# Performance work log

Measured on AMD Instinct MI355X. Metric: run time of the kernel, lower is better.

Reference implementation:

```python
import jax, jax.numpy as jnp
import numpy as np
from functools import partial

C = 10   # number of regular-repr fields
G = 4    # C4 rotation group order
EPS = 1e-5


def _lift_kernel(w):
    """Lifting (trivial->regular) P4 kernel. w: [C, Cin, k, k] ->
    full kernel [C*G, Cin, k, k] with output channel layout (field, orientation)."""
    ks = [jnp.rot90(w, r, axes=(-2, -1)) for r in range(G)]  # each [C,Cin,k,k]
    k = jnp.stack(ks, axis=1)                                 # [C,G,Cin,k,k]
    return k.reshape(w.shape[0] * G, w.shape[1], w.shape[2], w.shape[3])


def _gconv_kernel(w):
    """Regular->regular P4 kernel. w: [Cout, Cin, G, k, k] (indexed by relative
    input orientation) -> full kernel [Cout*G, Cin*G, k, k].
    K[co*G+r, ci*G+s] = rot90(w[co, ci, (s-r) mod G], r)."""
    Cout, Cin, _, k1, k2 = w.shape
    ks = []
    for r in range(G):
        wr = jnp.roll(w, shift=r, axis=2)             # wr[..., s, :, :] = w[..., (s-r)%G]
        wr = jnp.rot90(wr, r, axes=(-2, -1))          # rotate spatially by r*90deg
        ks.append(wr)
    k = jnp.stack(ks, axis=1)                          # [Cout, G, Cin, G, k, k]
    return k.reshape(Cout * G, Cin * G, k1, k2)


def _conv(x, k, pad):
    return jax.lax.conv_general_dilated(
        x, k, window_strides=(1, 1), padding=pad,
        dimension_numbers=('NCHW', 'OIHW', 'NCHW'))


def _bn_relu(x, gamma, beta):
    """InnerBatchNorm (stats shared over the G orientations of each field) + ReLU."""
    B, CG, H, W = x.shape
    xr = x.reshape(B, C, G, H, W)
    m = xr.mean(axis=(0, 2, 3, 4), keepdims=True)
    v = xr.var(axis=(0, 2, 3, 4), keepdims=True)
    g = gamma[None, :, None, None, None]
    b = beta[None, :, None, None, None]
    y = (xr - m) * jax.lax.rsqrt(v + EPS) * g + b
    return jnp.maximum(y.reshape(B, CG, H, W), 0.0)


def _maxpool2(x):
    return jax.lax.reduce_window(x, -jnp.inf, jax.lax.max,
                                 (1, 1, 2, 2), (1, 1, 2, 2), 'VALID')


def setup_inputs() -> dict:
    key = jax.random.key(0)
    ks = jax.random.split(key, 20)
    B = 1024
    x = jax.random.normal(ks[0], (B, 1, 28, 28), dtype=jnp.float32)
    w1 = jax.random.normal(ks[1], (C, 1, 3, 3), dtype=jnp.float32) * 0.3
    w2 = jax.random.normal(ks[2], (C, C, G, 3, 3), dtype=jnp.float32) * 0.1
    w3 = jax.random.normal(ks[3], (C, C, G, 3, 3), dtype=jnp.float32) * 0.1
    w4 = jax.random.normal(ks[4], (C, C, G, 3, 3), dtype=jnp.float32) * 0.1
    w5 = jax.random.normal(ks[5], (C, C, G, 3, 3), dtype=jnp.float32) * 0.1
    w6 = jax.random.normal(ks[6], (C, C, G, 3, 3), dtype=jnp.float32) * 0.1
    w7 = jax.random.normal(ks[7], (C, C, G, 4, 4), dtype=jnp.float32) * 0.1
    g1 = jnp.ones((C,), jnp.float32) + 0.1 * jax.random.normal(ks[8], (C,))
    b1 = 0.1 * jax.random.normal(ks[9], (C,))
    g2 = jnp.ones((C,), jnp.float32) + 0.1 * jax.random.normal(ks[10], (C,))
    b2 = 0.1 * jax.random.normal(ks[11], (C,))
    gs = jnp.ones((C,), jnp.float32) + 0.1 * jax.random.normal(ks[12], (C,))
    bs = 0.1 * jax.random.normal(ks[13], (C,))
    wfc = jax.random.normal(ks[14], (10, C * 11 * 11), dtype=jnp.float32) * 0.05
    bfc = jnp.zeros((10,), jnp.float32)
    return dict(x=x, w1=w1, w2=w2, w3=w3, w4=w4, w5=w5, w6=w6, w7=w7,
                g1=g1, b1=b1, g2=g2, b2=b2, gs=gs, bs=bs, wfc=wfc, bfc=bfc)


PAD1 = [(1, 1), (1, 1)]
PAD0 = [(0, 0), (0, 0)]


def reference(x, w1, w2, w3, w4, w5, w6, w7, g1, b1, g2, b2, gs, bs, wfc, bfc):
    # block1: lifting P4 conv 3x3 pad1 + InnerBN + ReLU  -> [B, 40, 28, 28]
    h = _bn_relu(_conv(x, _lift_kernel(w1), PAD1), g1, b1)
    # block2: P4 conv + BN + ReLU + 2x2 max pool         -> [B, 40, 14, 14]
    h = _maxpool2(_bn_relu(_conv(h, _gconv_kernel(w2), PAD1), g2, b2))
    # blocks 3-6: P4 conv + shared BN/ReLU               -> [B, 40, 14, 14]
    for w in (w3, w4, w5, w6):
        h = _bn_relu(_conv(h, _gconv_kernel(w), PAD1), gs, bs)
    # block7: P4 conv 4x4 pad0 + shared BN/ReLU          -> [B, 40, 11, 11]
    h = _bn_relu(_conv(h, _gconv_kernel(w7), PAD0), gs, bs)
    # group pooling: max over the G orientations of each field -> [B, 10, 11, 11]
    B = h.shape[0]
    h = h.reshape(B, C, G, 11, 11).max(axis=2)
    # fc
    return h.reshape(B, -1) @ wfc.T + bfc
```

## Files before the change

kernel.cpp:

```cpp
#include <hip/hip_runtime.h>

#define EPSV 1e-5f
#define INV28 (1.f / 3211264.f)
#define INV14 (1.f / 802816.f)
#define INV11 (1.f / 495616.f)

typedef __bf16 v8bf __attribute__((ext_vector_type(8)));
typedef _Float16 v8h __attribute__((ext_vector_type(8)));
typedef _Float16 v4h __attribute__((ext_vector_type(4)));
typedef float v4f __attribute__((ext_vector_type(4)));

__device__ __forceinline__ int rotsrc(int r, int dy, int dx, int K) {
  int sy, sx;
  if (r == 0)      { sy = dy;       sx = dx; }
  else if (r == 1) { sy = dx;       sx = K - 1 - dy; }
  else if (r == 2) { sy = K - 1 - dy; sx = K - 1 - dx; }
  else             { sy = K - 1 - dx; sx = dy; }
  return sy * K + sx;
}

__device__ __forceinline__ float gw_val(const float* __restrict__ w, int oc, int g,
                                        int j, int KS) {
  int tap = g / 5, cig = g % 5, ci = cig * 8 + j;
  int co = oc >> 2, r = oc & 3, cin = ci >> 2, s = ci & 3;
  int srel = (s - r) & 3;
  return w[((co * 10 + cin) * 4 + srel) * (KS * KS) + rotsrc(r, tap / KS, tap % KS, KS)];
}

__device__ __forceinline__ float stat8a(const float* __restrict__ p, int i) {
  float v = 0.f;
#pragma unroll
  for (int c = 0; c < 8; ++c)
    v += __hip_atomic_load(&p[c * 32 + i], __ATOMIC_RELAXED, __HIP_MEMORY_SCOPE_AGENT);
  return v;
}

__global__ void prep_kernel(const float* __restrict__ w1, const float* __restrict__ w2,
                            const float* __restrict__ w3, const float* __restrict__ w4,
                            const float* __restrict__ w5, const float* __restrict__ w6,
                            const float* __restrict__ w7,
                            float* __restrict__ K1, __bf16* __restrict__ Wb,
                            float* __restrict__ stats) {
  int idx = blockIdx.x * blockDim.x + threadIdx.x;
  if (idx < 1792) { stats[idx] = 0.f; return; }
  idx -= 1792;
  if (idx < 360) {
    int tap = idx / 40, oc = idx % 40;
    int c = oc >> 2, r = oc & 3;
    K1[idx] = w1[c * 9 + rotsrc(r, tap / 3, tap % 3, 3)];
    return;
  }
  idx -= 360;
  if (idx < 92160) {
    int l = idx / 18432, r0 = idx % 18432;
    const float* w = (l == 0) ? w2 : (l == 1) ? w3 : (l == 2) ? w4 : (l == 3) ? w5 : w6;
    int mt = r0 / 6144, r1 = r0 % 6144;
    int c = r1 / 512, r2 = r1 % 512;
    int q = r2 / 128, r3 = r2 % 128;
    int ocl = r3 / 8, j = r3 % 8;
    int oc = mt * 16 + ocl, g = c * 4 + q;
    float val = 0.f;
    if (oc < 40 && g < 45) val = gw_val(w, oc, g, j, 3);
    Wb[idx] = (__bf16)val;
    return;
  }
  idx -= 92160;
  if (idx < 30720) {
    int mt = idx / 10240, r1 = idx % 10240;
    int c = r1 / 512, r2 = r1 % 512;
    int q = r2 / 128, r3 = r2 % 128;
    int ocl = r3 / 8, j = r3 % 8;
    int oc = mt * 16 + ocl, g = c * 4 + q;
    float val = 0.f;
    if (oc < 40) val = gw_val(w7, oc, g, j, 4);
    Wb[92160 + idx] = (__bf16)val;
  }
}

__global__ __launch_bounds__(256) void conv1_stats(
    const float* __restrict__ x, const float* __restrict__ K1,
    float* __restrict__ stats) {
  __shared__ float ximg[900];
  __shared__ float wk[360];
  __shared__ float sstat[20];
  const int tid = threadIdx.x, img = blockIdx.x;
  if (tid < 20) sstat[tid] = 0.f;
  for (int i = tid; i < 900; i += 256) {
    int gy = i / 30 - 1, gx = i % 30 - 1;
    ximg[i] = (gy >= 0 && gy < 28 && gx >= 0 && gx < 28)
                  ? x[img * 784 + gy * 28 + gx] : 0.f;
  }
  for (int i = tid; i < 360; i += 256) wk[i] = K1[i];
  __syncthreads();

  float s[10], q[10];
#pragma unroll
  for (int f = 0; f < 10; ++f) { s[f] = 0.f; q[f] = 0.f; }
  for (int p = tid; p < 784; p += 256) {
    const int y = p / 28, xx = p % 28;
    float patch[9];
#pragma unroll
    for (int t = 0; t < 9; ++t) patch[t] = ximg[(y + t / 3) * 30 + xx + t % 3];
#pragma unroll
    for (int f = 0; f < 10; ++f) {
#pragma unroll
      for (int r = 0; r < 4; ++r) {
        const int oc = f * 4 + r;
        float v = 0.f;
#pragma unroll
        for (int t = 0; t < 9; ++t) v = fmaf(patch[t], wk[t * 40 + oc], v);
        s[f] += v; q[f] += v * v;
      }
    }
  }
#pragma unroll
  for (int f = 0; f < 10; ++f) {
#pragma unroll
    for (int off = 1; off <= 32; off <<= 1) {
      s[f] += __shfl_xor(s[f], off, 64);
      q[f] += __shfl_xor(q[f], off, 64);
    }
  }
  if ((tid & 63) == 0) {
#pragma unroll
    for (int f = 0; f < 10; ++f) {
      atomicAdd(&sstat[f], s[f]);
      atomicAdd(&sstat[10 + f], q[f]);
    }
  }
  __syncthreads();
  if (tid < 20) atomicAdd(&stats[(img & 7) * 32 + tid], sstat[tid]);
}

template<int R>
__global__ __launch_bounds__(256) void conv_band_fused(
    const float* __restrict__ x, const float* __restrict__ K1,
    const __bf16* __restrict__ Wl, const float* __restrict__ pstats,
    const float* __restrict__ pgamma, const float* __restrict__ pbeta,
    float pinvn, _Float16* __restrict__ T0, float* __restrict__ stats) {
  constexpr int NPIX = R * 28, NSUB = NPIX / 16, NSW = (NSUB + 3) / 4;
  constexpr int SROWS = R + 2, XR = R + 4;
  __shared__ __attribute__((aligned(16))) __bf16 tile[SROWS * 30 * 40];
  __shared__ float xpatch[XR * 32];
  __shared__ float wk[360];
  __shared__ float sc[10], sh[10], sstat[20];
  const int tid = threadIdx.x;
  int img, y0;
  if constexpr (R == 8) { img = blockIdx.x / 3; y0 = (blockIdx.x % 3) * 8; }
  else { img = blockIdx.x; y0 = 24; }

  if (tid < 20) sstat[tid] = 0.f;
  if (tid >= 32 && tid < 42) {
    int f = tid - 32;
    float mu = stat8a(pstats, f) * pinvn, q = stat8a(pstats, 10 + f) * pinvn;
    float isd = rsqrtf(q - mu * mu + EPSV);
    float s = pgamma[f] * isd;
    sc[f] = s; sh[f] = pbeta[f] - mu * s;
  }
  for (int i = tid; i < XR * 32; i += 256) {
    int gy = y0 - 2 + i / 32, gx = i % 32 - 2;
    xpatch[i] = (gy >= 0 && gy < 28 && gx >= 0 && gx < 28)
                    ? x[(long)img * 784 + gy * 28 + gx] : 0.f;
  }
  for (int i = tid; i < 360; i += 256) wk[i] = K1[i];
  __syncthreads();

  for (int p = tid; p < SROWS * 30; p += 256) {
    const int iy = p / 30, ix = p % 30;
    const int gy = y0 + iy - 1, gx = ix - 1;
    const bool inb = (gy >= 0 && gy < 28 && gx >= 0 && gx < 28);
    float patch[9];
#pragma unroll
    for (int t = 0; t < 9; ++t)
      patch[t] = xpatch[(iy + t / 3) * 32 + ix + t % 3];
    __bf16* tb = &tile[p * 40];
    if (inb) {
#pragma unroll 8
      for (int ci = 0; ci < 40; ++ci) {
        float v = 0.f;
#pragma unroll
        for (int t = 0; t < 9; ++t) v = fmaf(patch[t], wk[t * 40 + ci], v);
        v = fmaxf(0.f, fmaf(v, sc[ci >> 2], sh[ci >> 2]));
        tb[ci] = (__bf16)v;
      }
    } else {
#pragma unroll 8
      for (int ci = 0; ci < 40; ++ci) tb[ci] = (__bf16)0.f;
    }
  }
  __syncthreads();

  const int lane = tid & 63, wv = tid >> 6;
  const int m = lane & 15, quad = lane >> 4;
  int pbase[NSW], nsv[NSW];
  bool sv[NSW];
#pragma unroll
  for (int s = 0; s < NSW; ++s) {
    int ns = wv + 4 * s;
    sv[s] = ns < NSUB;
    int n = ns * 16 + m;
    n = n < NPIX ? n : NPIX - 1;
    nsv[s] = n;
    pbase[s] = ((n / 28) * 30 + (n % 28)) * 40;
  }
  v4f acc[3][NSW] = {};

  const __bf16* wlane = Wl + (quad * 16 + m) * 8;
  for (int c = 0; c < 12; ++c) {
    int g = 4 * c + quad; g = g > 44 ? 44 : g;
    int tap = g / 5, cig = g - tap * 5;
    int boff = ((tap / 3) * 30 + (tap % 3)) * 40 + cig * 8;
    v8bf bfr[NSW];
#pragma unroll
    for (int s = 0; s < NSW; ++s)
      if (sv[s]) bfr[s] = *(const v8bf*)&tile[pbase[s] + boff];
    v8bf afr[3];
#pragma unroll
    for (int mt = 0; mt < 3; ++mt)
      afr[mt] = *(const v8bf*)(wlane + (mt * 12 + c) * 512);
#pragma unroll
    for (int s = 0; s < NSW; ++s)
      if (sv[s]) {
#pragma unroll
        for (int mt = 0; mt < 3; ++mt)
          acc[mt][s] = __builtin_amdgcn_mfma_f32_16x16x32_bf16(afr[mt], bfr[s],
                                                              acc[mt][s], 0, 0, 0);
      }
  }

#pragma unroll
  for (int mt = 0; mt < 3; ++mt) {
    float svv = 0.f, qvv = 0.f;
#pragma unroll
    for (int s = 0; s < NSW; ++s)
      if (sv[s]) {
#pragma unroll
        for (int r = 0; r < 4; ++r) { float v = acc[mt][s][r]; svv += v; qvv += v * v; }
      }
    const bool ocok = (mt < 2) || (quad < 2);
#pragma unroll
    for (int off = 1; off <= 8; off <<= 1) {
      svv += __shfl_xor(svv, off, 64);
      qvv += __shfl_xor(qvv, off, 64);
    }
    if (m == 0 && ocok) {
      atomicAdd(&sstat[mt * 4 + quad], svv);
      atomicAdd(&sstat[10 + mt * 4 + quad], qvv);
    }
  }

  __syncthreads();
  __bf16* pool = tile;
#pragma unroll
  for (int mt = 0; mt < 3; ++mt) {
    const bool ocok = (mt < 2) || (quad < 2);
    const int oc0 = mt * 16 + quad * 4;
#pragma unroll
    for (int s = 0; s < NSW; ++s)
      if (ocok && sv[s]) {
#pragma unroll
        for (int r = 0; r < 4; ++r)
          pool[(oc0 + r) * NPIX + nsv[s]] = (__bf16)acc[mt][s][r];
      }
  }
  __syncthreads();
  constexpr int PR = R / 2, PCNT = 40 * PR * 14;
  for (int i = tid; i < PCNT; i += 256) {
    int oc = i / (PR * 14), rem = i % (PR * 14);
    int py = rem / 14, px = rem % 14;
    const __bf16* pp = pool + oc * NPIX + py * 56 + px * 2;
    float a = (float)pp[0], b = (float)pp[1], c = (float)pp[28], d = (float)pp[29];
    T0[((long)img * 256 + (y0 / 2 + py + 1) * 16 + (px + 1)) * 40 + oc] =
        (_Float16)fmaxf(fmaxf(a, b), fmaxf(c, d));
  }
  if (tid < 20) atomicAdd(&stats[(img & 7) * 32 + tid], sstat[tid]);
}

__global__ __launch_bounds__(256) void conv_tile(
    const _Float16* __restrict__ Tin, const __bf16* __restrict__ Wl,
    const float* __restrict__ pstats, const float* __restrict__ pg,
    const float* __restrict__ pb, float pinvn,
    _Float16* __restrict__ Tout, float* __restrict__ stG) {
  __shared__ __attribute__((aligned(16))) __bf16 tile[256 * 40];
  __shared__ float sc[10], sh[10], sstat[20];
  const int tid = threadIdx.x, img = blockIdx.x;
  const int lane = tid & 63, wv = tid >> 6;
  const int m = lane & 15, quad = lane >> 4;
  if (tid < 20) sstat[tid] = 0.f;
  if (tid >= 32 && tid < 42) {
    int f = tid - 32;
    float mu = stat8a(pstats, f) * pinvn, q = stat8a(pstats, 10 + f) * pinvn;
    float isd = rsqrtf(q - mu * mu + EPSV);
    float s = pg[f] * isd;
    sc[f] = s; sh[f] = pb[f] - mu * s;
  }
  __syncthreads();
  {
    const int iy = tid >> 4, ix = tid & 15;
    const bool border = (iy == 0) | (iy == 15) | (ix == 0) | (ix == 15);
    const _Float16* src = Tin + ((long)img * 256 + tid) * 40;
    __bf16* dst = &tile[tid * 40];
#pragma unroll
    for (int cg5 = 0; cg5 < 5; ++cg5) {
      v8bf pk;
      if (!border) {
        v8h rv = *(const v8h*)(src + cg5 * 8);
#pragma unroll
        for (int u = 0; u < 8; ++u) {
          const int f = (cg5 * 8 + u) >> 2;
          pk[u] = (__bf16)fmaxf(0.f, fmaf((float)rv[u], sc[f], sh[f]));
        }
      } else {
#pragma unroll
        for (int u = 0; u < 8; ++u) pk[u] = (__bf16)0.f;
      }
      *(v8bf*)(dst + cg5 * 8) = pk;
    }
  }
  __syncthreads();

  int pb3[4], n3[4];
  bool sv3[4], va3[4];
#pragma unroll
  for (int s = 0; s < 4; ++s) {
    int ns = wv + 4 * s;
    sv3[s] = ns < 13;
    int n = ns * 16 + m;
    va3[s] = sv3[s] && (n < 196);
    n = n < 196 ? n : 195;
    n3[s] = n;
    pb3[s] = ((n / 14) * 16 + (n % 14)) * 40;
  }
  const int wofs = (quad * 16 + m) * 8;
  v4f acc[3][4];
#pragma unroll
  for (int mt = 0; mt < 3; ++mt)
#pragma unroll
    for (int s = 0; s < 4; ++s) acc[mt][s] = (v4f){0.f, 0.f, 0.f, 0.f};
  for (int c = 0; c < 12; ++c) {
    int g = 4 * c + quad; g = g > 44 ? 44 : g;
    int tap = g / 5, cig = g - tap * 5;
    int boff = ((tap / 3) * 16 + (tap % 3)) * 40 + cig * 8;
    v8bf bfr[4];
#pragma unroll
    for (int s = 0; s < 4; ++s)
      if (sv3[s]) bfr[s] = *(const v8bf*)&tile[pb3[s] + boff];
    v8bf afr[3];
#pragma unroll
    for (int mt = 0; mt < 3; ++mt)
      afr[mt] = *(const v8bf*)(Wl + wofs + (mt * 12 + c) * 512);
#pragma unroll
    for (int s = 0; s < 4; ++s)
      if (sv3[s]) {
#pragma unroll
        for (int mt = 0; mt < 3; ++mt)
          acc[mt][s] = __builtin_amdgcn_mfma_f32_16x16x32_bf16(afr[mt], bfr[s],
                                                              acc[mt][s], 0, 0, 0);
      }
  }

#pragma unroll
  for (int mt = 0; mt < 3; ++mt) {
    float svv = 0.f, qvv = 0.f;
#pragma unroll
    for (int s = 0; s < 4; ++s)
      if (va3[s]) {
#pragma unroll
        for (int r = 0; r < 4; ++r) { float v = acc[mt][s][r]; svv += v; qvv += v * v; }
      }
    const bool ocok = (mt < 2) || (quad < 2);
#pragma unroll
    for (int off = 1; off <= 8; off <<= 1) {
      svv += __shfl_xor(svv, off, 64);
      qvv += __shfl_xor(qvv, off, 64);
    }
    if (m == 0 && ocok) {
      atomicAdd(&sstat[mt * 4 + quad], svv);
      atomicAdd(&sstat[10 + mt * 4 + quad], qvv);
    }
  }
  __syncthreads();
  if (tid < 20) atomicAdd(&stG[(img & 7) * 32 + tid], sstat[tid]);

#pragma unroll
  for (int mt = 0; mt < 3; ++mt) {
    const bool ocok = (mt < 2) || (quad < 2);
    if (!ocok) continue;
#pragma unroll
    for (int s = 0; s < 4; ++s)
      if (va3[s]) {
        v4h pk;
#pragma unroll
        for (int r = 0; r < 4; ++r) pk[r] = (_Float16)acc[mt][s][r];
        const int n = n3[s];
        *(v4h*)(Tout + ((long)img * 256 + (n / 14 + 1) * 16 + (n % 14 + 1)) * 40
                + mt * 16 + quad * 4) = pk;
      }
  }
}

__global__ __launch_bounds__(256) void conv7_tile(
    const _Float16* __restrict__ Tin, const __bf16* __restrict__ Wl,
    const float* __restrict__ pstats, const float* __restrict__ pg,
    const float* __restrict__ pb,
    _Float16* __restrict__ T7, float* __restrict__ stG) {
  __shared__ __attribute__((aligned(16))) __bf16 tile[256 * 40];
  __shared__ float sc[10], sh[10], sstat[20];
  const int tid = threadIdx.x, img = blockIdx.x;
  const int lane = tid & 63, wv = tid >> 6;
  const int m = lane & 15, quad = lane >> 4;
  if (tid < 20) sstat[tid] = 0.f;
  if (tid >= 32 && tid < 42) {
    int f = tid - 32;
    float mu = stat8a(pstats, f) * INV14, q = stat8a(pstats, 10 + f) * INV14;
    float isd = rsqrtf(q - mu * mu + EPSV);
    float s = pg[f] * isd;
    sc[f] = s; sh[f] = pb[f] - mu * s;
  }
  __syncthreads();
  {
    const int iy = tid >> 4, ix = tid & 15;
    const bool border = (iy == 0) | (iy == 15) | (ix == 0) | (ix == 15);
    const _Float16* src = Tin + ((long)img * 256 + tid) * 40;
    __bf16* dst = &tile[tid * 40];
#pragma unroll
    for (int cg5 = 0; cg5 < 5; ++cg5) {
      v8bf pk;
      if (!border) {
        v8h rv = *(const v8h*)(src + cg5 * 8);
#pragma unroll
        for (int u = 0; u < 8; ++u) {
          const int f = (cg5 * 8 + u) >> 2;
          pk[u] = (__bf16)fmaxf(0.f, fmaf((float)rv[u], sc[f], sh[f]));
        }
      } else {
#pragma unroll
        for (int u = 0; u < 8; ++u) pk[u] = (__bf16)0.f;
      }
      *(v8bf*)(dst + cg5 * 8) = pk;
    }
  }
  __syncthreads();

  int pb7[2], n7[2];
  bool va7[2];
#pragma unroll
  for (int s = 0; s < 2; ++s) {
    int ns = wv + 4 * s;
    int n = ns * 16 + m;
    va7[s] = n < 121;
    n = n < 121 ? n : 120;
    n7[s] = n;
    pb7[s] = ((n / 11 + 1) * 16 + (n % 11 + 1)) * 40;
  }
  const int wofs = (quad * 16 + m) * 8;
  v4f acc[3][2];
#pragma unroll
  for (int mt = 0; mt < 3; ++mt)
#pragma unroll
    for (int s = 0; s < 2; ++s) acc[mt][s] = (v4f){0.f, 0.f, 0.f, 0.f};
  for (int c = 0; c < 20; ++c) {
    int g = 4 * c + quad;
    int tap = g / 5, cig = g - tap * 5;
    int boff = ((tap >> 2) * 16 + (tap & 3)) * 40 + cig * 8;
    v8bf bfr[2];
#pragma unroll
    for (int s = 0; s < 2; ++s) bfr[s] = *(const v8bf*)&tile[pb7[s] + boff];
    v8bf afr[3];
#pragma unroll
    for (int mt = 0; mt < 3; ++mt)
      afr[mt] = *(const v8bf*)(Wl + wofs + (mt * 20 + c) * 512);
#pragma unroll
    for (int s = 0; s < 2; ++s)
#pragma unroll
      for (int mt = 0; mt < 3; ++mt)
        acc[mt][s] = __builtin_amdgcn_mfma_f32_16x16x32_bf16(afr[mt], bfr[s],
                                                            acc[mt][s], 0, 0, 0);
  }

#pragma unroll
  for (int mt = 0; mt < 3; ++mt) {
    float svv = 0.f, qvv = 0.f;
#pragma unroll
    for (int s = 0; s < 2; ++s)
      if (va7[s]) {
#pragma unroll
        for (int r = 0; r < 4; ++r) { float v = acc[mt][s][r]; svv += v; qvv += v * v; }
      }
    const bool ocok = (mt < 2) || (quad < 2);
#pragma unroll
    for (int off = 1; off <= 8; off <<= 1) {
      svv += __shfl_xor(svv, off, 64);
      qvv += __shfl_xor(qvv, off, 64);
    }
    if (m == 0 && ocok) {
      atomicAdd(&sstat[mt * 4 + quad], svv);
      atomicAdd(&sstat[10 + mt * 4 + quad], qvv);
    }
  }
  __syncthreads();
  if (tid < 20) atomicAdd(&stG[(img & 7) * 32 + tid], sstat[tid]);

#pragma unroll
  for (int mt = 0; mt < 3; ++mt) {
    const bool ocok = (mt < 2) || (quad < 2);
    if (!ocok) continue;
#pragma unroll
    for (int s = 0; s < 2; ++s)
      if (va7[s]) {
        v4h pk;
#pragma unroll
        for (int r = 0; r < 4; ++r) pk[r] = (_Float16)acc[mt][s][r];
        *(v4h*)(T7 + ((long)img * 121 + n7[s]) * 40 + mt * 16 + quad * 4) = pk;
      }
  }
}

__global__ __launch_bounds__(256) void head_kernel(
    const _Float16* __restrict__ T7, const float* __restrict__ stats7,
    const float* __restrict__ gs, const float* __restrict__ bs,
    const float* __restrict__ wfc, const float* __restrict__ bfc,
    float* __restrict__ out) {
  __shared__ float sc[10], sh[10];
  __shared__ float mbuf[1210];
  __shared__ float red[40];
  const int tid = threadIdx.x, img = blockIdx.x;
  if (tid < 10) {
    float mu = stat8a(stats7, tid) * INV11, q = stat8a(stats7, 10 + tid) * INV11;
    float isd = rsqrtf(q - mu * mu + EPSV);
    float s = gs[tid] * isd;
    sc[tid] = s;
    sh[tid] = bs[tid] - mu * s;
  }
  __syncthreads();
  for (int p = tid; p < 121; p += 256) {
    const _Float16* rp = T7 + ((long)img * 121 + p) * 40;
#pragma unroll
    for (int cg5 = 0; cg5 < 5; ++cg5) {
      v8h v = *(const v8h*)(rp + cg5 * 8);
#pragma unroll
      for (int fh = 0; fh < 2; ++fh) {
        const int f = cg5 * 2 + fh;
        float mx = fmaf((float)v[fh * 4], sc[f], sh[f]);
#pragma unroll
        for (int r = 1; r < 4; ++r)
          mx = fmaxf(mx, fmaf((float)v[fh * 4 + r], sc[f], sh[f]));
        mbuf[f * 121 + p] = fmaxf(0.f, mx);
      }
    }
  }
  __syncthreads();
  const int wv = tid >> 6;
  for (int k = 0; k < 10; ++k) {
    float p = 0.f;
    for (int j = tid; j < 1210; j += 256) p = fmaf(mbuf[j], wfc[k * 1210 + j], p);
#pragma unroll
    for (int off = 32; off > 0; off >>= 1) p += __shfl_xor(p, off, 64);
    if ((tid & 63) == 0) red[k * 4 + wv] = p;
  }
  __syncthreads();
  if (tid < 10)
    out[img * 10 + tid] = bfc[tid] + red[tid * 4] + red[tid * 4 + 1] +
                          red[tid * 4 + 2] + red[tid * 4 + 3];
}

extern "C" void kernel_launch(void* const* d_in, const int* in_sizes, int n_in,
                              void* d_out, int out_size, void* d_ws, size_t ws_size,
                              hipStream_t stream) {
  const float* x   = (const float*)d_in[0];
  const float* w1  = (const float*)d_in[1];
  const float* w2  = (const float*)d_in[2];
  const float* w3  = (const float*)d_in[3];
  const float* w4  = (const float*)d_in[4];
  const float* w5  = (const float*)d_in[5];
  const float* w6  = (const float*)d_in[6];
  const float* w7  = (const float*)d_in[7];
  const float* g1  = (const float*)d_in[8];
  const float* b1  = (const float*)d_in[9];
  const float* g2  = (const float*)d_in[10];
  const float* b2  = (const float*)d_in[11];
  const float* gs  = (const float*)d_in[12];
  const float* bs  = (const float*)d_in[13];
  const float* wfc = (const float*)d_in[14];
  const float* bfc = (const float*)d_in[15];

  float* ws = (float*)d_ws;
  float* K1    = ws;
  float* stats = ws + 360;
  __bf16* Wb   = (__bf16*)(ws + 2152);
  _Float16* T0 = (_Float16*)(ws + 63592);
  _Float16* T1 = (_Float16*)(ws + 5306472L);
  _Float16* T7 = (_Float16*)(ws + 10549352L);

  prep_kernel<<<489, 256, 0, stream>>>(w1, w2, w3, w4, w5, w6, w7, K1, Wb, stats);
  conv1_stats<<<1024, 256, 0, stream>>>(x, K1, stats);
  conv_band_fused<8><<<3072, 256, 0, stream>>>(x, K1, Wb, stats, g1, b1, INV28,
                                               T0, stats + 256);
  conv_band_fused<4><<<1024, 256, 0, stream>>>(x, K1, Wb, stats, g1, b1, INV28,
                                               T0, stats + 256);
  conv_tile<<<1024, 256, 0, stream>>>(T0, Wb + 18432, stats + 256, g2, b2, INV28,
                                      T1, stats + 512);
  conv_tile<<<1024, 256, 0, stream>>>(T1, Wb + 36864, stats + 512, gs, bs, INV14,
                                      T0, stats + 768);
  conv_tile<<<1024, 256, 0, stream>>>(T0, Wb + 55296, stats + 768, gs, bs, INV14,
                                      T1, stats + 1024);
  conv_tile<<<1024, 256, 0, stream>>>(T1, Wb + 73728, stats + 1024, gs, bs, INV14,
                                      T0, stats + 1280);
  conv7_tile<<<1024, 256, 0, stream>>>(T0, Wb + 92160, stats + 1280, gs, bs,
                                       T7, stats + 1536);
  head_kernel<<<1024, 256, 0, stream>>>(T7, stats + 1536, gs, bs, wfc, bfc,
                                        (float*)d_out);
}
```

Baseline: 319.5 us.

## Recompute lifting conv with fp16 MFMA and switch all gconv operands to fp16

The scalar FMA loop that recomputed the lifting conv (block1) inside the fused band kernel is replaced by an MFMA-based im2col of 9 taps zero-padded to 32, using a new packed fp16 weight matrix built in the prep kernel. All bf16 tiles, weights and MFMA calls become fp16, which also removes the fp16-to-bf16 conversion when tiles are staged. This offloads the per-pixel 360-FMA recompute to the matrix cores and shrinks shared memory. In exchange, fp16 has less exponent range than bf16, and the MFMA wastes most of its K dimension.

```diff
diff --git a/kernel.cpp b/kernel.cpp
--- a/kernel.cpp
+++ b/kernel.cpp
@@ -5,7 +5,6 @@
 #define INV14 (1.f / 802816.f)
 #define INV11 (1.f / 495616.f)
 
-typedef __bf16 v8bf __attribute__((ext_vector_type(8)));
 typedef _Float16 v8h __attribute__((ext_vector_type(8)));
 typedef _Float16 v4h __attribute__((ext_vector_type(4)));
 typedef float v4f __attribute__((ext_vector_type(4)));
@@ -39,7 +38,7 @@
                             const float* __restrict__ w3, const float* __restrict__ w4,
                             const float* __restrict__ w5, const float* __restrict__ w6,
                             const float* __restrict__ w7,
-                            float* __restrict__ K1, __bf16* __restrict__ Wb,
+                            float* __restrict__ K1, _Float16* __restrict__ Wb,
                             float* __restrict__ stats) {
   int idx = blockIdx.x * blockDim.x + threadIdx.x;
   if (idx < 1792) { stats[idx] = 0.f; return; }
@@ -61,7 +60,7 @@
     int oc = mt * 16 + ocl, g = c * 4 + q;
     float val = 0.f;
     if (oc < 40 && g < 45) val = gw_val(w, oc, g, j, 3);
-    Wb[idx] = (__bf16)val;
+    Wb[idx] = (_Float16)val;
     return;
   }
   idx -= 92160;
@@ -73,7 +72,19 @@
     int oc = mt * 16 + ocl, g = c * 4 + q;
     float val = 0.f;
     if (oc < 40) val = gw_val(w7, oc, g, j, 4);
-    Wb[92160 + idx] = (__bf16)val;
+    Wb[92160 + idx] = (_Float16)val;
+    return;
+  }
+  idx -= 30720;
+  if (idx < 1536) {
+    int mt = idx / 512, r1 = idx % 512;
+    int q = r1 / 128, r2 = r1 % 128;
+    int ocl = r2 / 8, j = r2 % 8;
+    int oc = mt * 16 + ocl, k = q * 8 + j;
+    float val = 0.f;
+    if (oc < 40 && k < 9)
+      val = w1[(oc >> 2) * 9 + rotsrc(oc & 3, k / 3, k % 3, 3)];
+    Wb[122880 + idx] = (_Float16)val;
   }
 }
 
@@ -134,15 +145,15 @@
 
 template<int R>
 __global__ __launch_bounds__(256) void conv_band_fused(
-    const float* __restrict__ x, const float* __restrict__ K1,
-    const __bf16* __restrict__ Wl, const float* __restrict__ pstats,
+    const float* __restrict__ x, const _Float16* __restrict__ W1m,
+    const _Float16* __restrict__ Wl, const float* __restrict__ pstats,
     const float* __restrict__ pgamma, const float* __restrict__ pbeta,
     float pinvn, _Float16* __restrict__ T0, float* __restrict__ stats) {
   constexpr int NPIX = R * 28, NSUB = NPIX / 16, NSW = (NSUB + 3) / 4;
   constexpr int SROWS = R + 2, XR = R + 4;
-  __shared__ __attribute__((aligned(16))) __bf16 tile[SROWS * 30 * 40];
-  __shared__ float xpatch[XR * 32];
-  __shared__ float wk[360];
+  constexpr int NPIX_S = SROWS * 30, NSUB_S = (NPIX_S + 15) / 16;
+  __shared__ __attribute__((aligned(16))) _Float16 tile[SROWS * 30 * 40];
+  __shared__ _Float16 xpatch[XR * 32];
   __shared__ float sc[10], sh[10], sstat[20];
   const int tid = threadIdx.x;
   int img, y0;
@@ -159,39 +170,59 @@
   }
   for (int i = tid; i < XR * 32; i += 256) {
     int gy = y0 - 2 + i / 32, gx = i % 32 - 2;
-    xpatch[i] = (gy >= 0 && gy < 28 && gx >= 0 && gx < 28)
-                    ? x[(long)img * 784 + gy * 28 + gx] : 0.f;
-  }
-  for (int i = tid; i < 360; i += 256) wk[i] = K1[i];
-  __syncthreads();
-
-  for (int p = tid; p < SROWS * 30; p += 256) {
-    const int iy = p / 30, ix = p % 30;
-    const int gy = y0 + iy - 1, gx = ix - 1;
-    const bool inb = (gy >= 0 && gy < 28 && gx >= 0 && gx < 28);
-    float patch[9];
-#pragma unroll
-    for (int t = 0; t < 9; ++t)
-      patch[t] = xpatch[(iy + t / 3) * 32 + ix + t % 3];
-    __bf16* tb = &tile[p * 40];
-    if (inb) {
-#pragma unroll 8
-      for (int ci = 0; ci < 40; ++ci) {
-        float v = 0.f;
-#pragma unroll
-        for (int t = 0; t < 9; ++t) v = fmaf(patch[t], wk[t * 40 + ci], v);
-        v = fmaxf(0.f, fmaf(v, sc[ci >> 2], sh[ci >> 2]));
-        tb[ci] = (__bf16)v;
-      }
-    } else {
-#pragma unroll 8
-      for (int ci = 0; ci < 40; ++ci) tb[ci] = (__bf16)0.f;
-    }
+    float v = (gy >= 0 && gy < 28 && gx >= 0 && gx < 28)
+                  ? x[(long)img * 784 + gy * 28 + gx] : 0.f;
+    xpatch[i] = (_Float16)v;
   }
   __syncthreads();
 
   const int lane = tid & 63, wv = tid >> 6;
   const int m = lane & 15, quad = lane >> 4;
+
+  {
+    v8h a1[3];
+#pragma unroll
+    for (int mt = 0; mt < 3; ++mt)
+      a1[mt] = *(const v8h*)(W1m + mt * 512 + (quad * 16 + m) * 8);
+    for (int ns = wv; ns < NSUB_S; ns += 4) {
+      const int n = ns * 16 + m;
+      const bool valid = n < NPIX_S;
+      const int nc = valid ? n : NPIX_S - 1;
+      const int iy = nc / 30, ix = nc % 30;
+      v8h bfr;
+#pragma unroll
+      for (int j = 0; j < 8; ++j) bfr[j] = (_Float16)0.f;
+      if (quad < 2) {
+#pragma unroll
+        for (int j = 0; j < 8; ++j) {
+          const int k = quad * 8 + j;
+          if (k < 9) bfr[j] = xpatch[(iy + k / 3) * 32 + (ix + k % 3)];
+        }
+      }
+      v4f cfr[3];
+#pragma unroll
+      for (int mt = 0; mt < 3; ++mt)
+        cfr[mt] = __builtin_amdgcn_mfma_f32_16x16x32_f16(
+            a1[mt], bfr, (v4f){0.f, 0.f, 0.f, 0.f}, 0, 0, 0);
+      const int gy = y0 + iy - 1, gx = ix - 1;
+      const bool inb = (gy >= 0 && gy < 28 && gx >= 0 && gx < 28);
+#pragma unroll
+      for (int mt = 0; mt < 3; ++mt) {
+        if (mt == 2 && quad >= 2) continue;
+        const int f = mt * 4 + quad;
+        const float scf = sc[f], shf = sh[f];
+        v4h pk;
+#pragma unroll
+        for (int r = 0; r < 4; ++r) {
+          float v = inb ? fmaxf(0.f, fmaf(cfr[mt][r], scf, shf)) : 0.f;
+          pk[r] = (_Float16)v;
+        }
+        if (valid) *(v4h*)&tile[nc * 40 + mt * 16 + quad * 4] = pk;
+      }
+    }
+  }
+  __syncthreads();
+
   int pbase[NSW], nsv[NSW];
   bool sv[NSW];
 #pragma unroll
@@ -205,26 +236,26 @@
   }
   v4f acc[3][NSW] = {};
 
-  const __bf16* wlane = Wl + (quad * 16 + m) * 8;
+  const _Float16* wlane = Wl + (quad * 16 + m) * 8;
   for (int c = 0; c < 12; ++c) {
     int g = 4 * c + quad; g = g > 44 ? 44 : g;
     int tap = g / 5, cig = g - tap * 5;
     int boff = ((tap / 3) * 30 + (tap % 3)) * 40 + cig * 8;
-    v8bf bfr[NSW];
+    v8h bfr[NSW];
 #pragma unroll
     for (int s = 0; s < NSW; ++s)
-      if (sv[s]) bfr[s] = *(const v8bf*)&tile[pbase[s] + boff];
-    v8bf afr[3];
+      if (sv[s]) bfr[s] = *(const v8h*)&tile[pbase[s] + boff];
+    v8h afr[3];
 #pragma unroll
     for (int mt = 0; mt < 3; ++mt)
-      afr[mt] = *(const v8bf*)(wlane + (mt * 12 + c) * 512);
+      afr[mt] = *(const v8h*)(wlane + (mt * 12 + c) * 512);
 #pragma unroll
     for (int s = 0; s < NSW; ++s)
       if (sv[s]) {
 #pragma unroll
         for (int mt = 0; mt < 3; ++mt)
-          acc[mt][s] = __builtin_amdgcn_mfma_f32_16x16x32_bf16(afr[mt], bfr[s],
-                                                              acc[mt][s], 0, 0, 0);
+          acc[mt][s] = __builtin_amdgcn_mfma_f32_16x16x32_f16(afr[mt], bfr[s],
+                                                             acc[mt][s], 0, 0, 0);
       }
   }
 
@@ -250,7 +281,7 @@
   }
 
   __syncthreads();
-  __bf16* pool = tile;
+  _Float16* pool = tile;
 #pragma unroll
   for (int mt = 0; mt < 3; ++mt) {
     const bool ocok = (mt < 2) || (quad < 2);
@@ -260,7 +291,7 @@
       if (ocok && sv[s]) {
 #pragma unroll
         for (int r = 0; r < 4; ++r)
-          pool[(oc0 + r) * NPIX + nsv[s]] = (__bf16)acc[mt][s][r];
+          pool[(oc0 + r) * NPIX + nsv[s]] = (_Float16)acc[mt][s][r];
       }
   }
   __syncthreads();
@@ -268,7 +299,7 @@
   for (int i = tid; i < PCNT; i += 256) {
     int oc = i / (PR * 14), rem = i % (PR * 14);
     int py = rem / 14, px = rem % 14;
-    const __bf16* pp = pool + oc * NPIX + py * 56 + px * 2;
+    const _Float16* pp = pool + oc * NPIX + py * 56 + px * 2;
     float a = (float)pp[0], b = (float)pp[1], c = (float)pp[28], d = (float)pp[29];
     T0[((long)img * 256 + (y0 / 2 + py + 1) * 16 + (px + 1)) * 40 + oc] =
         (_Float16)fmaxf(fmaxf(a, b), fmaxf(c, d));
@@ -277,11 +308,11 @@
 }
 
 __global__ __launch_bounds__(256) void conv_tile(
-    const _Float16* __restrict__ Tin, const __bf16* __restrict__ Wl,
+    const _Float16* __restrict__ Tin, const _Float16* __restrict__ Wl,
     const float* __restrict__ pstats, const float* __restrict__ pg,
     const float* __restrict__ pb, float pinvn,
     _Float16* __restrict__ Tout, float* __restrict__ stG) {
-  __shared__ __attribute__((aligned(16))) __bf16 tile[256 * 40];
+  __shared__ __attribute__((aligned(16))) _Float16 tile[256 * 40];
   __shared__ float sc[10], sh[10], sstat[20];
   const int tid = threadIdx.x, img = blockIdx.x;
   const int lane = tid & 63, wv = tid >> 6;
@@ -299,22 +330,22 @@
     const int iy = tid >> 4, ix = tid & 15;
     const bool border = (iy == 0) | (iy == 15) | (ix == 0) | (ix == 15);
     const _Float16* src = Tin + ((long)img * 256 + tid) * 40;
-    __bf16* dst = &tile[tid * 40];
+    _Float16* dst = &tile[tid * 40];
 #pragma unroll
     for (int cg5 = 0; cg5 < 5; ++cg5) {
-      v8bf pk;
+      v8h pk;
       if (!border) {
         v8h rv = *(const v8h*)(src + cg5 * 8);
 #pragma unroll
         for (int u = 0; u < 8; ++u) {
           const int f = (cg5 * 8 + u) >> 2;
-          pk[u] = (__bf16)fmaxf(0.f, fmaf((float)rv[u], sc[f], sh[f]));
+          pk[u] = (_Float16)fmaxf(0.f, fmaf((float)rv[u], sc[f], sh[f]));
         }
       } else {
 #pragma unroll
-        for (int u = 0; u < 8; ++u) pk[u] = (__bf16)0.f;
-      }
-      *(v8bf*)(dst + cg5 * 8) = pk;
+        for (int u = 0; u < 8; ++u) pk[u] = (_Float16)0.f;
+      }
+      *(v8h*)(dst + cg5 * 8) = pk;
     }
   }
   __syncthreads();
@@ -341,21 +372,21 @@
     int g = 4 * c + quad; g = g > 44 ? 44 : g;
     int tap = g / 5, cig = g - tap * 5;
     int boff = ((tap / 3) * 16 + (tap % 3)) * 40 + cig * 8;
-    v8bf bfr[4];
+    v8h bfr[4];
 #pragma unroll
     for (int s = 0; s < 4; ++s)
-      if (sv3[s]) bfr[s] = *(const v8bf*)&tile[pb3[s] + boff];
-    v8bf afr[3];
+      if (sv3[s]) bfr[s] = *(const v8h*)&tile[pb3[s] + boff];
+    v8h afr[3];
 #pragma unroll
     for (int mt = 0; mt < 3; ++mt)
-      afr[mt] = *(const v8bf*)(Wl + wofs + (mt * 12 + c) * 512);
+      afr[mt] = *(const v8h*)(Wl + wofs + (mt * 12 + c) * 512);
 #pragma unroll
     for (int s = 0; s < 4; ++s)
       if (sv3[s]) {
 #pragma unroll
         for (int mt = 0; mt < 3; ++mt)
-          acc[mt][s] = __builtin_amdgcn_mfma_f32_16x16x32_bf16(afr[mt], bfr[s],
-                                                              acc[mt][s], 0, 0, 0);
+          acc[mt][s] = __builtin_amdgcn_mfma_f32_16x16x32_f16(afr[mt], bfr[s],
+                                                             acc[mt][s], 0, 0, 0);
       }
   }
 
@@ -400,11 +431,11 @@
 }
 
 __global__ __launch_bounds__(256) void conv7_tile(
-    const _Float16* __restrict__ Tin, const __bf16* __restrict__ Wl,
+    const _Float16* __restrict__ Tin, const _Float16* __restrict__ Wl,
     const float* __restrict__ pstats, const float* __restrict__ pg,
     const float* __restrict__ pb,
     _Float16* __restrict__ T7, float* __restrict__ stG) {
-  __shared__ __attribute__((aligned(16))) __bf16 tile[256 * 40];
+  __shared__ __attribute__((aligned(16))) _Float16 tile[256 * 40];
   __shared__ float sc[10], sh[10], sstat[20];
   const int tid = threadIdx.x, img = blockIdx.x;
   const int lane = tid & 63, wv = tid >> 6;
@@ -422,22 +453,22 @@
     const int iy = tid >> 4, ix = tid & 15;
     const bool border = (iy == 0) | (iy == 15) | (ix == 0) | (ix == 15);
     const _Float16* src = Tin + ((long)img * 256 + tid) * 40;
-    __bf16* dst = &tile[tid * 40];
+    _Float16* dst = &tile[tid * 40];
 #pragma unroll
     for (int cg5 = 0; cg5 < 5; ++cg5) {
-      v8bf pk;
+      v8h pk;
       if (!border) {
         v8h rv = *(const v8h*)(src + cg5 * 8);
 #pragma unroll
         for (int u = 0; u < 8; ++u) {
           const int f = (cg5 * 8 + u) >> 2;
-          pk[u] = (__bf16)fmaxf(0.f, fmaf((float)rv[u], sc[f], sh[f]));
+          pk[u] = (_Float16)fmaxf(0.f, fmaf((float)rv[u], sc[f], sh[f]));
         }
       } else {
 #pragma unroll
-        for (int u = 0; u < 8; ++u) pk[u] = (__bf16)0.f;
-      }
-      *(v8bf*)(dst + cg5 * 8) = pk;
+        for (int u = 0; u < 8; ++u) pk[u] = (_Float16)0.f;
+      }
+      *(v8h*)(dst + cg5 * 8) = pk;
     }
   }
   __syncthreads();
@@ -463,19 +494,19 @@
     int g = 4 * c + quad;
     int tap = g / 5, cig = g - tap * 5;
     int boff = ((tap >> 2) * 16 + (tap & 3)) * 40 + cig * 8;
-    v8bf bfr[2];
-#pragma unroll
-    for (int s = 0; s < 2; ++s) bfr[s] = *(const v8bf*)&tile[pb7[s] + boff];
-    v8bf afr[3];
+    v8h bfr[2];
+#pragma unroll
+    for (int s = 0; s < 2; ++s) bfr[s] = *(const v8h*)&tile[pb7[s] + boff];
+    v8h afr[3];
 #pragma unroll
     for (int mt = 0; mt < 3; ++mt)
-      afr[mt] = *(const v8bf*)(Wl + wofs + (mt * 20 + c) * 512);
+      afr[mt] = *(const v8h*)(Wl + wofs + (mt * 20 + c) * 512);
 #pragma unroll
     for (int s = 0; s < 2; ++s)
 #pragma unroll
       for (int mt = 0; mt < 3; ++mt)
-        acc[mt][s] = __builtin_amdgcn_mfma_f32_16x16x32_bf16(afr[mt], bfr[s],
-                                                            acc[mt][s], 0, 0, 0);
+        acc[mt][s] = __builtin_amdgcn_mfma_f32_16x16x32_f16(afr[mt], bfr[s],
+                                                           acc[mt][s], 0, 0, 0);
   }
 
 #pragma unroll
@@ -585,18 +616,19 @@
   const float* bfc = (const float*)d_in[15];
 
   float* ws = (float*)d_ws;
-  float* K1    = ws;
-  float* stats = ws + 360;
-  __bf16* Wb   = (__bf16*)(ws + 2152);
-  _Float16* T0 = (_Float16*)(ws + 63592);
-  _Float16* T1 = (_Float16*)(ws + 5306472L);
-  _Float16* T7 = (_Float16*)(ws + 10549352L);
-
-  prep_kernel<<<489, 256, 0, stream>>>(w1, w2, w3, w4, w5, w6, w7, K1, Wb, stats);
+  float* K1      = ws;
+  float* stats   = ws + 360;
+  _Float16* Wb   = (_Float16*)(ws + 2152);
+  _Float16* W1m  = Wb + 122880;
+  _Float16* T0   = (_Float16*)(ws + 64360);
+  _Float16* T1   = (_Float16*)(ws + 5307240L);
+  _Float16* T7   = (_Float16*)(ws + 10550120L);
+
+  prep_kernel<<<495, 256, 0, stream>>>(w1, w2, w3, w4, w5, w6, w7, K1, Wb, stats);
   conv1_stats<<<1024, 256, 0, stream>>>(x, K1, stats);
-  conv_band_fused<8><<<3072, 256, 0, stream>>>(x, K1, Wb, stats, g1, b1, INV28,
+  conv_band_fused<8><<<3072, 256, 0, stream>>>(x, W1m, Wb, stats, g1, b1, INV28,
                                                T0, stats + 256);
-  conv_band_fused<4><<<1024, 256, 0, stream>>>(x, K1, Wb, stats, g1, b1, INV28,
+  conv_band_fused<4><<<1024, 256, 0, stream>>>(x, W1m, Wb, stats, g1, b1, INV28,
                                                T0, stats + 256);
   conv_tile<<<1024, 256, 0, stream>>>(T0, Wb + 18432, stats + 256, g2, b2, INV28,
                                       T1, stats + 512);
```

Measured after the change: 321.4 us. Within noise of the previous version (+0.6%).
